# Performance work log

Measured on AMD Instinct MI355X. Metric: run time of the kernel, lower is better.

The kernel has to match this reference:

```python
import jax, jax.numpy as jnp
import numpy as np

N = 100000   # nodes
E = 1600000  # edges
G = 2048     # graphs
IN = 128     # in_channels
H = 128      # hidden_channels
L = 3        # num GIN layers


def setup_inputs() -> dict:
    key = jax.random.key(0)
    ks = jax.random.split(key, 16)
    s = 0.05
    rn = lambda k, shp: s * jax.random.normal(k, shp, dtype=jnp.float32)
    return {
        "x": jax.random.normal(ks[0], (N, IN), dtype=jnp.float32),
        "edge_index": jax.random.randint(ks[1], (2, E), 0, N, dtype=jnp.int32),
        "batch": jnp.sort(jax.random.randint(ks[2], (N,), 0, G, dtype=jnp.int32)),
        # encoder input projection
        "W_in": rn(ks[3], (IN, H)), "b_in": jnp.zeros((H,), jnp.float32),
        # GIN layers: MLP = Linear(H,H)-ReLU-Linear(H,H), learnable eps
        "Ws1": rn(ks[4], (L, H, H)), "bs1": jnp.zeros((L, H), jnp.float32),
        "Ws2": rn(ks[5], (L, H, H)), "bs2": jnp.zeros((L, H), jnp.float32),
        "eps": jnp.zeros((L,), jnp.float32),
        # encoder output projection (out_channels == hidden_channels)
        "W_out": rn(ks[6], (H, H)), "b_out": jnp.zeros((H,), jnp.float32),
        # decoder: Linear(H, H//2) - ReLU - Linear(H//2, IN)
        "Wd1": rn(ks[7], (H, H // 2)), "bd1": jnp.zeros((H // 2,), jnp.float32),
        "Wd2": rn(ks[8], (H // 2, IN)), "bd2": jnp.zeros((IN,), jnp.float32),
    }


def reference(x, edge_index, batch, W_in, b_in, Ws1, bs1, Ws2, bs2, eps,
              W_out, b_out, Wd1, bd1, Wd2, bd2):
    src, dst = edge_index[0], edge_index[1]
    # input projection
    h = jax.nn.relu(x @ W_in + b_in)                      # [N, H]
    # GIN message passing (sum aggregation)
    for l in range(L):
        agg = jax.ops.segment_sum(h[src], dst, num_segments=N)   # [N, H]
        z = (1.0 + eps[l]) * h + agg
        m = jax.nn.relu(z @ Ws1[l] + bs1[l]) @ Ws2[l] + bs2[l]
        h = jax.nn.relu(m)
    # global mean pool per graph
    pooled = jax.ops.segment_sum(h, batch, num_segments=G)       # [G, H]
    counts = jax.ops.segment_sum(jnp.ones((N,), h.dtype), batch, num_segments=G)
    pooled = pooled / jnp.maximum(counts, 1.0)[:, None]
    graph_embeddings = pooled @ W_out + b_out                    # [G, H]
    # gather graph embedding back to each node, then decode
    node_embeddings = graph_embeddings[batch]                    # [N, H]
    reconstructed = jax.nn.relu(node_embeddings @ Wd1 + bd1) @ Wd2 + bd2  # [N, IN]
    return reconstructed, graph_embeddings
```

## Files before the change

kernel.cpp:

```cpp
#include <hip/hip_runtime.h>

typedef unsigned int uint;
typedef unsigned short ushort;
typedef __attribute__((ext_vector_type(8))) short bf16x8;
typedef __attribute__((ext_vector_type(4))) float f32x4;

constexpr int N_ = 100000;
constexpr int E_ = 1600000;
constexpr int G_ = 2048;
constexpr int H_ = 128;
constexpr int WPSZ = 16384;
constexpr int NSLICE = 8;
constexpr int SL_SZ = N_ / NSLICE;
constexpr int SL_BLOCKS = 256;
constexpr int CAP = 64;

__device__ inline ushort f2bf(float f) {
    uint u = __builtin_bit_cast(uint, f);
    u += 0x7fffu + ((u >> 16) & 1u);
    return (ushort)(u >> 16);
}
__device__ inline float bflo(uint v) { return __builtin_bit_cast(float, v << 16); }
__device__ inline float bfhi(uint v) { return __builtin_bit_cast(float, v & 0xffff0000u); }

__global__ __launch_bounds__(256) void k_fill_c(const int* __restrict__ srcv, const int* __restrict__ dstv,
                                                int* __restrict__ cnt, int* __restrict__ csr_src) {
    int slice = blockIdx.x & (NSLICE - 1);
    int grp   = blockIdx.x >> 3;
    int lo = slice * SL_SZ, hi = lo + SL_SZ;
    int stride = SL_BLOCKS * 256;
    for (int e = grp * 256 + threadIdx.x; e < E_; e += stride) {
        int d = __builtin_nontemporal_load(&dstv[e]);
        if (d >= lo && d < hi) {
            int s = __builtin_nontemporal_load(&srcv[e]);
            int slot = atomicAdd(&cnt[d], 1);
            if (slot < CAP) csr_src[(size_t)d * CAP + slot] = s;
        }
    }
}

__global__ __launch_bounds__(64) void k_pack(const float* __restrict__ W, ushort* __restrict__ Wp) {
    int lane = threadIdx.x;
    int n = ((blockIdx.x >> 2) * 16) + (lane & 15);
    int k0 = (blockIdx.x & 3) * 32 + (lane >> 4) * 8;
    bf16x8 v;
    #pragma unroll
    for (int j = 0; j < 8; j++) v[j] = (short)f2bf(W[(size_t)(k0 + j) * H_ + n]);
    *(bf16x8*)&Wp[(size_t)(blockIdx.x * 64 + lane) * 8] = v;
}

template <bool F32IN, bool RELU>
__global__ __launch_bounds__(256) void k_mm(const void* __restrict__ in, const ushort* __restrict__ Wp,
                                            const float* __restrict__ bias, ushort* __restrict__ out, int M) {
    __shared__ ushort lW[WPSZ];
    int t = threadIdx.x;
    #pragma unroll
    for (int i = 0; i < 8; i++) {
        int idx = i * 256 + t;
        *(bf16x8*)&lW[(size_t)idx * 8] = *(const bf16x8*)&Wp[(size_t)idx * 8];
    }
    __syncthreads();

    int wave = t >> 6, lane = t & 63;
    int col = lane & 15, kc = lane >> 4;
    int row0 = blockIdx.x * 128 + wave * 32;

    float bv[8];
    #pragma unroll
    for (int nt = 0; nt < 8; nt++) bv[nt] = bias[nt * 16 + col];

    f32x4 acc[2][8];
    #pragma unroll
    for (int rt = 0; rt < 2; rt++)
        #pragma unroll
        for (int nt = 0; nt < 8; nt++) {
            acc[rt][nt][0] = bv[nt]; acc[rt][nt][1] = bv[nt];
            acc[rt][nt][2] = bv[nt]; acc[rt][nt][3] = bv[nt];
        }

    #pragma unroll
    for (int kb = 0; kb < 4; kb++) {
        bf16x8 bf[8];
        #pragma unroll
        for (int nt = 0; nt < 8; nt++)
            bf[nt] = *(const bf16x8*)&lW[(size_t)(((nt * 4 + kb) * 64) + lane) * 8];
        #pragma unroll
        for (int rt = 0; rt < 2; rt++) {
            int r = row0 + rt * 16 + col;
            if (r > M - 1) r = M - 1;
            bf16x8 af;
            if (F32IN) {
                const float* fin = (const float*)in;
                float4 a0 = *(const float4*)&fin[(size_t)r * H_ + kb * 32 + kc * 8];
                float4 a1 = *(const float4*)&fin[(size_t)r * H_ + kb * 32 + kc * 8 + 4];
                af[0] = (short)f2bf(a0.x); af[1] = (short)f2bf(a0.y);
                af[2] = (short)f2bf(a0.z); af[3] = (short)f2bf(a0.w);
                af[4] = (short)f2bf(a1.x); af[5] = (short)f2bf(a1.y);
                af[6] = (short)f2bf(a1.z); af[7] = (short)f2bf(a1.w);
            } else {
                af = *(const bf16x8*)&((const ushort*)in)[(size_t)r * H_ + kb * 32 + kc * 8];
            }
            #pragma unroll
            for (int nt = 0; nt < 8; nt++)
                acc[rt][nt] = __builtin_amdgcn_mfma_f32_16x16x32_bf16(af, bf[nt], acc[rt][nt], 0, 0, 0);
        }
    }

    #pragma unroll
    for (int rt = 0; rt < 2; rt++) {
        int rbase = row0 + rt * 16 + kc * 4;
        #pragma unroll
        for (int r = 0; r < 4; r++) {
            int row = rbase + r;
            if (row < M) {
                #pragma unroll
                for (int nt = 0; nt < 8; nt++) {
                    float f = acc[rt][nt][r];
                    if (RELU) f = fmaxf(f, 0.f);
                    out[(size_t)row * H_ + nt * 16 + col] = f2bf(f);
                }
            }
        }
    }
}

__global__ __launch_bounds__(256) void k_agg(const uint* __restrict__ h, const int* __restrict__ cnt,
                                             const int* __restrict__ csr_src, const float* __restrict__ eps,
                                             int layer, uint* __restrict__ z) {
    int node = blockIdx.x * 4 + (threadIdx.x >> 6);
    int c = threadIdx.x & 63;
    int deg = cnt[node];
    if (deg > CAP) deg = CAP;
    const int* cs = csr_src + (size_t)node * CAP;
    float a0 = 0.f, a1 = 0.f;
    int j = 0;
    for (; j + 4 <= deg; j += 4) {
        int s0 = cs[j], s1 = cs[j + 1], s2 = cs[j + 2], s3 = cs[j + 3];
        uint v0 = h[(size_t)s0 * 64 + c];
        uint v1 = h[(size_t)s1 * 64 + c];
        uint v2 = h[(size_t)s2 * 64 + c];
        uint v3 = h[(size_t)s3 * 64 + c];
        a0 += bflo(v0) + bflo(v1) + bflo(v2) + bflo(v3);
        a1 += bfhi(v0) + bfhi(v1) + bfhi(v2) + bfhi(v3);
    }
    for (; j < deg; j++) {
        uint v = h[(size_t)cs[j] * 64 + c];
        a0 += bflo(v); a1 += bfhi(v);
    }
    float e1 = 1.0f + eps[layer];
    uint hv = h[(size_t)node * 64 + c];
    float o0 = fmaf(e1, bflo(hv), a0);
    float o1 = fmaf(e1, bfhi(hv), a1);
    z[(size_t)node * 64 + c] = (uint)f2bf(o0) | ((uint)f2bf(o1) << 16);
}

template <int KDIM, int NDIM, bool RELU>
__global__ __launch_bounds__(256) void k_lin(const float* __restrict__ in, const float* __restrict__ W,
                                             const float* __restrict__ bias, float* __restrict__ out) {
    constexpr int CV = NDIM / 4;
    constexpr int RPI = 256 / CV;
    constexpr int R = 4;
    constexpr int ROWS = RPI * R;
    __shared__ float4 Wl[KDIM * CV];
    for (int i = threadIdx.x; i < KDIM * CV; i += 256) Wl[i] = ((const float4*)W)[i];
    __syncthreads();

    int cv = threadIdx.x % CV;
    int rg = threadIdx.x / CV;
    int row0 = blockIdx.x * ROWS + rg * R;

    float4 bv = ((const float4*)bias)[cv];
    float4 acc[R];
    #pragma unroll
    for (int r = 0; r < R; r++) acc[r] = bv;

    const float4* in4 = (const float4*)in;
    #pragma unroll 2
    for (int k4 = 0; k4 < KDIM / 4; k4++) {
        float4 w0 = Wl[(4 * k4 + 0) * CV + cv];
        float4 w1 = Wl[(4 * k4 + 1) * CV + cv];
        float4 w2 = Wl[(4 * k4 + 2) * CV + cv];
        float4 w3 = Wl[(4 * k4 + 3) * CV + cv];
        #pragma unroll
        for (int r = 0; r < R; r++) {
            float4 a = in4[(size_t)(row0 + r) * (KDIM / 4) + k4];
            acc[r].x = fmaf(a.x, w0.x, fmaf(a.y, w1.x, fmaf(a.z, w2.x, fmaf(a.w, w3.x, acc[r].x))));
            acc[r].y = fmaf(a.x, w0.y, fmaf(a.y, w1.y, fmaf(a.z, w2.y, fmaf(a.w, w3.y, acc[r].y))));
            acc[r].z = fmaf(a.x, w0.z, fmaf(a.y, w1.z, fmaf(a.z, w2.z, fmaf(a.w, w3.z, acc[r].z))));
            acc[r].w = fmaf(a.x, w0.w, fmaf(a.y, w1.w, fmaf(a.z, w2.w, fmaf(a.w, w3.w, acc[r].w))));
        }
    }
    #pragma unroll
    for (int r = 0; r < R; r++) {
        float4 o = acc[r];
        if (RELU) {
            o.x = fmaxf(o.x, 0.f); o.y = fmaxf(o.y, 0.f);
            o.z = fmaxf(o.z, 0.f); o.w = fmaxf(o.w, 0.f);
        }
        ((float4*)out)[(size_t)(row0 + r) * CV + cv] = o;
    }
}

__global__ __launch_bounds__(64) void k_pool(const uint* __restrict__ h2, const int* __restrict__ batch,
                                             float* __restrict__ pooled, float* __restrict__ gcnt, int n) {
    int c = threadIdx.x;
    int base = blockIdx.x * 128;
    int nmax = min(base + 128, n);
    int gcur = batch[base];
    float a0 = 0.f, a1 = 0.f;
    int run = 0;
    for (int i = base; i < nmax; i++) {
        int g = batch[i];
        if (g != gcur) {
            atomicAdd(&pooled[(size_t)gcur * 128 + 2 * c], a0);
            atomicAdd(&pooled[(size_t)gcur * 128 + 2 * c + 1], a1);
            if (c == 0) atomicAdd(&gcnt[gcur], (float)run);
            a0 = 0.f; a1 = 0.f; run = 0; gcur = g;
        }
        uint v = h2[(size_t)i * 64 + c];
        a0 += bflo(v); a1 += bfhi(v);
        run++;
    }
    atomicAdd(&pooled[(size_t)gcur * 128 + 2 * c], a0);
    atomicAdd(&pooled[(size_t)gcur * 128 + 2 * c + 1], a1);
    if (c == 0) atomicAdd(&gcnt[gcur], (float)run);
}

__global__ __launch_bounds__(256) void k_div(float* __restrict__ pooled, const float* __restrict__ gcnt) {
    int i = blockIdx.x * 256 + threadIdx.x;
    float cnt = fmaxf(gcnt[i >> 7], 1.0f);
    pooled[i] = pooled[i] / cnt;
}

__global__ __launch_bounds__(256) void k_scatter(const float* __restrict__ recong, const int* __restrict__ batch,
                                                 float* __restrict__ out) {
    int i = blockIdx.x * 256 + threadIdx.x;
    int node = i >> 5;
    int c4 = i & 31;
    int g = batch[node];
    ((float4*)out)[(size_t)node * 32 + c4] = ((const float4*)recong)[(size_t)g * 32 + c4];
}


extern "C" void kernel_launch(void* const* d_in, const int* in_sizes, int n_in,
                              void* d_out, int out_size, void* d_ws, size_t ws_size,
                              hipStream_t stream) {
    const float* x     = (const float*)d_in[0];
    const int*   ei    = (const int*)d_in[1];
    const int*   batch = (const int*)d_in[2];
    const float* W_in  = (const float*)d_in[3];
    const float* b_in  = (const float*)d_in[4];
    const float* Ws1   = (const float*)d_in[5];
    const float* bs1   = (const float*)d_in[6];
    const float* Ws2   = (const float*)d_in[7];
    const float* bs2   = (const float*)d_in[8];
    const float* eps   = (const float*)d_in[9];
    const float* W_out = (const float*)d_in[10];
    const float* b_out = (const float*)d_in[11];
    const float* Wd1   = (const float*)d_in[12];
    const float* bd1   = (const float*)d_in[13];
    const float* Wd2   = (const float*)d_in[14];
    const float* bd2   = (const float*)d_in[15];

    const int* srcv = ei;
    const int* dstv = ei + E_;

    char* ws = (char*)d_ws;
    size_t off = 0;
    auto nextp = [&](size_t bytes) -> char* {
        char* p = ws + off;
        off += (bytes + 255) & ~(size_t)255;
        return p;
    };
    ushort* buf0    = (ushort*)nextp((size_t)N_ * H_ * 2);
    ushort* buf1    = (ushort*)nextp((size_t)N_ * H_ * 2);
    ushort* Wp      = (ushort*)nextp((size_t)7 * WPSZ * 2);
    int*   cnt      = (int*)nextp((size_t)N_ * 4);
    int*   csr_src  = (int*)nextp((size_t)N_ * CAP * 4);
    float* pooled   = (float*)nextp((size_t)G_ * H_ * 4);
    float* gcnt     = (float*)nextp((size_t)G_ * 4);
    float* tg       = (float*)nextp((size_t)G_ * 64 * 4);
    float* recong   = (float*)nextp((size_t)G_ * H_ * 4);

    float* out_recon = (float*)d_out;
    float* out_ge    = (float*)d_out + (size_t)N_ * H_;

    hipMemsetAsync(cnt, 0, (size_t)N_ * 4, stream);
    hipMemsetAsync(pooled, 0, (size_t)G_ * H_ * 4, stream);
    hipMemsetAsync(gcnt, 0, (size_t)G_ * 4, stream);

    k_fill_c<<<NSLICE * SL_BLOCKS, 256, 0, stream>>>(srcv, dstv, cnt, csr_src);

    k_pack<<<32, 64, 0, stream>>>(W_in, Wp + 0 * WPSZ);
    for (int l = 0; l < 3; l++) {
        k_pack<<<32, 64, 0, stream>>>(Ws1 + (size_t)l * H_ * H_, Wp + (size_t)(1 + 2 * l) * WPSZ);
        k_pack<<<32, 64, 0, stream>>>(Ws2 + (size_t)l * H_ * H_, Wp + (size_t)(2 + 2 * l) * WPSZ);
    }

    int mmgrid = (N_ + 127) / 128;

    k_mm<true, true><<<mmgrid, 256, 0, stream>>>(x, Wp, b_in, buf0, N_);

    ushort* hb = buf0;
    ushort* ob = buf1;
    for (int l = 0; l < 3; l++) {
        k_agg<<<N_ / 4, 256, 0, stream>>>((const uint*)hb, cnt, csr_src, eps, l, (uint*)ob);
        k_mm<false, true><<<mmgrid, 256, 0, stream>>>(ob, Wp + (size_t)(1 + 2 * l) * WPSZ, bs1 + l * H_, hb, N_);
        k_mm<false, true><<<mmgrid, 256, 0, stream>>>(hb, Wp + (size_t)(2 + 2 * l) * WPSZ, bs2 + l * H_, ob, N_);
        ushort* tmp = hb; hb = ob; ob = tmp;
    }

    k_pool<<<(N_ + 127) / 128, 64, 0, stream>>>((const uint*)hb, batch, pooled, gcnt, N_);
    k_div<<<G_ * H_ / 256, 256, 0, stream>>>(pooled, gcnt);
    k_lin<128, 128, false><<<G_ / 32, 256, 0, stream>>>(pooled, W_out, b_out, out_ge);

    k_lin<128, 64, true><<<G_ / 64, 256, 0, stream>>>(out_ge, Wd1, bd1, tg);
    k_lin<64, 128, false><<<G_ / 32, 256, 0, stream>>>(tg, Wd2, bd2, recong);
    k_scatter<<<(size_t)N_ * 32 / 256, 256, 0, stream>>>(recong, batch, out_recon);
}
```

Before: 616.5 us.

## Vectorize edge loads, stage GEMM output through LDS, widen aggregation unroll

The CSR fill kernel now reads src/dst as 4-wide int vectors, cutting load instruction count. The matmul epilogue writes results to a padded LDS tile and then stores full 16-byte rows coalesced, instead of scattered 2-byte stores. The aggregation loop is unrolled by 8 with vectorized index loads to raise memory-level parallelism. The LDS buffer grows, which may lower occupancy, and an extra barrier is added.

```diff
diff --git a/kernel.cpp b/kernel.cpp
--- a/kernel.cpp
+++ b/kernel.cpp
@@ -4,6 +4,7 @@
 typedef unsigned short ushort;
 typedef __attribute__((ext_vector_type(8))) short bf16x8;
 typedef __attribute__((ext_vector_type(4))) float f32x4;
+typedef __attribute__((ext_vector_type(4))) int int4v;
 
 constexpr int N_ = 100000;
 constexpr int E_ = 1600000;
@@ -14,6 +15,7 @@
 constexpr int SL_SZ = N_ / NSLICE;
 constexpr int SL_BLOCKS = 256;
 constexpr int CAP = 64;
+constexpr int CLDS = 136;
 
 __device__ inline ushort f2bf(float f) {
     uint u = __builtin_bit_cast(uint, f);
@@ -29,12 +31,20 @@
     int grp   = blockIdx.x >> 3;
     int lo = slice * SL_SZ, hi = lo + SL_SZ;
     int stride = SL_BLOCKS * 256;
-    for (int e = grp * 256 + threadIdx.x; e < E_; e += stride) {
-        int d = __builtin_nontemporal_load(&dstv[e]);
-        if (d >= lo && d < hi) {
-            int s = __builtin_nontemporal_load(&srcv[e]);
-            int slot = atomicAdd(&cnt[d], 1);
-            if (slot < CAP) csr_src[(size_t)d * CAP + slot] = s;
+    const int4v* d4 = (const int4v*)dstv;
+    const int4v* s4 = (const int4v*)srcv;
+    int nq = E_ / 4;
+    for (int q = grp * 256 + threadIdx.x; q < nq; q += stride) {
+        int4v d = __builtin_nontemporal_load(&d4[q]);
+        int4v s = __builtin_nontemporal_load(&s4[q]);
+        #pragma unroll
+        for (int k = 0; k < 4; k++) {
+            int dd = d[k];
+            int ss = s[k];
+            if (dd >= lo && dd < hi) {
+                int slot = atomicAdd(&cnt[dd], 1);
+                if (slot < CAP) csr_src[(size_t)dd * CAP + slot] = ss;
+            }
         }
     }
 }
@@ -52,12 +62,12 @@
 template <bool F32IN, bool RELU>
 __global__ __launch_bounds__(256) void k_mm(const void* __restrict__ in, const ushort* __restrict__ Wp,
                                             const float* __restrict__ bias, ushort* __restrict__ out, int M) {
-    __shared__ ushort lW[WPSZ];
+    __shared__ ushort sm[128 * CLDS];
     int t = threadIdx.x;
     #pragma unroll
     for (int i = 0; i < 8; i++) {
         int idx = i * 256 + t;
-        *(bf16x8*)&lW[(size_t)idx * 8] = *(const bf16x8*)&Wp[(size_t)idx * 8];
+        *(bf16x8*)&sm[(size_t)idx * 8] = *(const bf16x8*)&Wp[(size_t)idx * 8];
     }
     __syncthreads();
 
@@ -83,7 +93,7 @@
         bf16x8 bf[8];
         #pragma unroll
         for (int nt = 0; nt < 8; nt++)
-            bf[nt] = *(const bf16x8*)&lW[(size_t)(((nt * 4 + kb) * 64) + lane) * 8];
+            bf[nt] = *(const bf16x8*)&sm[(size_t)(((nt * 4 + kb) * 64) + lane) * 8];
         #pragma unroll
         for (int rt = 0; rt < 2; rt++) {
             int r = row0 + rt * 16 + col;
@@ -106,20 +116,30 @@
         }
     }
 
+    __syncthreads();
     #pragma unroll
     for (int rt = 0; rt < 2; rt++) {
-        int rbase = row0 + rt * 16 + kc * 4;
+        int rl0 = wave * 32 + rt * 16 + kc * 4;
         #pragma unroll
         for (int r = 0; r < 4; r++) {
-            int row = rbase + r;
-            if (row < M) {
-                #pragma unroll
-                for (int nt = 0; nt < 8; nt++) {
-                    float f = acc[rt][nt][r];
-                    if (RELU) f = fmaxf(f, 0.f);
-                    out[(size_t)row * H_ + nt * 16 + col] = f2bf(f);
-                }
+            #pragma unroll
+            for (int nt = 0; nt < 8; nt++) {
+                float f = acc[rt][nt][r];
+                if (RELU) f = fmaxf(f, 0.f);
+                sm[(size_t)(rl0 + r) * CLDS + nt * 16 + col] = f2bf(f);
             }
+        }
+    }
+    __syncthreads();
+
+    int base_row = blockIdx.x * 128;
+    #pragma unroll
+    for (int i = 0; i < 8; i++) {
+        int ch = i * 256 + t;
+        int row = ch >> 4, part = ch & 15;
+        if (base_row + row < M) {
+            bf16x8 v = *(const bf16x8*)&sm[(size_t)row * CLDS + part * 8];
+            *(bf16x8*)&out[(size_t)(base_row + row) * H_ + part * 8] = v;
         }
     }
 }
@@ -134,12 +154,26 @@
     const int* cs = csr_src + (size_t)node * CAP;
     float a0 = 0.f, a1 = 0.f;
     int j = 0;
+    for (; j + 8 <= deg; j += 8) {
+        int4v i0 = *(const int4v*)&cs[j];
+        int4v i1 = *(const int4v*)&cs[j + 4];
+        uint v0 = h[(size_t)i0[0] * 64 + c];
+        uint v1 = h[(size_t)i0[1] * 64 + c];
+        uint v2 = h[(size_t)i0[2] * 64 + c];
+        uint v3 = h[(size_t)i0[3] * 64 + c];
+        uint v4 = h[(size_t)i1[0] * 64 + c];
+        uint v5 = h[(size_t)i1[1] * 64 + c];
+        uint v6 = h[(size_t)i1[2] * 64 + c];
+        uint v7 = h[(size_t)i1[3] * 64 + c];
+        a0 += bflo(v0) + bflo(v1) + bflo(v2) + bflo(v3) + bflo(v4) + bflo(v5) + bflo(v6) + bflo(v7);
+        a1 += bfhi(v0) + bfhi(v1) + bfhi(v2) + bfhi(v3) + bfhi(v4) + bfhi(v5) + bfhi(v6) + bfhi(v7);
+    }
     for (; j + 4 <= deg; j += 4) {
-        int s0 = cs[j], s1 = cs[j + 1], s2 = cs[j + 2], s3 = cs[j + 3];
-        uint v0 = h[(size_t)s0 * 64 + c];
-        uint v1 = h[(size_t)s1 * 64 + c];
-        uint v2 = h[(size_t)s2 * 64 + c];
-        uint v3 = h[(size_t)s3 * 64 + c];
+        int4v i0 = *(const int4v*)&cs[j];
+        uint v0 = h[(size_t)i0[0] * 64 + c];
+        uint v1 = h[(size_t)i0[1] * 64 + c];
+        uint v2 = h[(size_t)i0[2] * 64 + c];
+        uint v3 = h[(size_t)i0[3] * 64 + c];
         a0 += bflo(v0) + bflo(v1) + bflo(v2) + bflo(v3);
         a1 += bfhi(v0) + bfhi(v1) + bfhi(v2) + bfhi(v3);
     }
@@ -285,9 +319,9 @@
     float* out_recon = (float*)d_out;
     float* out_ge    = (float*)d_out + (size_t)N_ * H_;
 
-    hipMemsetAsync(cnt, 0, (size_t)N_ * 4, stream);
-    hipMemsetAsync(pooled, 0, (size_t)G_ * H_ * 4, stream);
-    hipMemsetAsync(gcnt, 0, (size_t)G_ * 4, stream);
+    (void)hipMemsetAsync(cnt, 0, (size_t)N_ * 4, stream);
+    (void)hipMemsetAsync(pooled, 0, (size_t)G_ * H_ * 4, stream);
+    (void)hipMemsetAsync(gcnt, 0, (size_t)G_ * 4, stream);
 
     k_fill_c<<<NSLICE * SL_BLOCKS, 256, 0, stream>>>(srcv, dstv, cnt, csr_src);
 
```

Result: no change. 618.8 us (+0.4%).
